# Kernel optimization log

Measured on AMD Instinct MI355X. Metric: run time of the kernel, lower is better.

## Reference

```python
import jax, jax.numpy as jnp
import numpy as np


def setup_inputs() -> dict:
    key = jax.random.key(0)
    k1, k2 = jax.random.split(key)
    N, D, K = 131072, 256, 1024
    x = jax.random.normal(k1, (N, D), dtype=jnp.float32)
    centroids = jax.random.normal(k2, (K, D), dtype=jnp.float32)
    return {"x": x, "centroids": centroids}


def reference(x, centroids):
    """Nearest-centroid assignment with euclidean similarity (kmeans_pytorch euc_sim):
        sim[n,k] = 2 * x[n] . c[k] - |x[n]|^2 - |c[k]|^2  ( = -||x[n]-c[k]||^2 )
    Returns (max_sim [N], labels [N]).
    """
    # [N, K] similarity via single GEMM plus broadcast norms
    sim = (2.0 * jnp.einsum('nd,kd->nk', x, centroids)
           - jnp.sum(x * x, axis=-1, keepdims=True)
           - jnp.sum(centroids * centroids, axis=-1)[None, :])
    max_sim = jnp.max(sim, axis=-1)
    labels = jnp.argmax(sim, axis=-1)
    return max_sim, labels
```

## Files before the change

kernel.cpp:

```cpp
#include <hip/hip_runtime.h>

constexpr int N = 131072;
constexpr int D = 256;
constexpr int K = 1024;

constexpr int TM = 128;
constexpr int TK = 128;
constexpr float EPS = 0.08f;

typedef _Float16 f16x8 __attribute__((ext_vector_type(8)));
typedef float f32x4 __attribute__((ext_vector_type(4)));

__device__ _Float16 g_ctile[66 * 8192];

__device__ __forceinline__ float sqf(float a) { return __fmul_rn(a, a); }

__device__ __forceinline__ float np_sumsq128(const float* q) {
    float lane[16];
#pragma unroll
    for (int j = 0; j < 16; j++) {
        const float r0 = __fadd_rn(sqf(q[j]),      sqf(q[64 + j]));
        const float r1 = __fadd_rn(sqf(q[16 + j]), sqf(q[80 + j]));
        const float r2 = __fadd_rn(sqf(q[32 + j]), sqf(q[96 + j]));
        const float r3 = __fadd_rn(sqf(q[48 + j]), sqf(q[112 + j]));
        lane[j] = __fadd_rn(__fadd_rn(r0, r1), __fadd_rn(r2, r3));
    }
    float t[8];
#pragma unroll
    for (int i = 0; i < 8; i++) t[i] = __fadd_rn(lane[i], lane[i + 8]);
    float u[4];
#pragma unroll
    for (int i = 0; i < 4; i++) u[i] = __fadd_rn(t[i], t[i + 4]);
    return __fadd_rn(__fadd_rn(u[0], u[2]), __fadd_rn(u[1], u[3]));
}
__device__ __forceinline__ float np_pw256_sq(const float* p) {
    return __fadd_rn(np_sumsq128(p), np_sumsq128(p + 128));
}

__device__ __forceinline__ float np_dot256(const float* a, const float* b) {
    float A[4] = {0.f, 0.f, 0.f, 0.f};
#pragma unroll 4
    for (int t = 0; t < 16; t++) {
#pragma unroll
        for (int i = 3; i >= 0; i--) {
            const int base = 16 * t + 4 * i;
#pragma unroll
            for (int j = 0; j < 4; j++)
                A[j] = __fadd_rn(A[j], __fmul_rn(a[base + j], b[base + j]));
        }
    }
    return __fadd_rn(__fadd_rn(A[0], A[1]), __fadd_rn(A[2], A[3]));
}

#define SPL(vec, comp, he, le, idx)                                  \
    {                                                                \
        const float fv_ = (vec).comp;                                \
        const _Float16 hh_ = (_Float16)fv_;                          \
        he[idx] = hh_;                                               \
        le[idx] = (_Float16)(fv_ - (float)hh_);                      \
    }

__global__ __launch_bounds__(256) void prep_kernel(const float* __restrict__ c,
                                                   float* __restrict__ cn) {
    const int idx = blockIdx.x * 256 + threadIdx.x;
    const int kglob = idx >> 5;
    const int dslot = idx & 31;
    const int dc = dslot >> 2, kg = dslot & 3;
    const float* src = c + (size_t)kglob * D + dc * 32 + kg * 8;
    const float4 s0 = ((const float4*)src)[0];
    const float4 s1 = ((const float4*)src)[1];
    f16x8 h, l;
    SPL(s0, x, h, l, 0) SPL(s0, y, h, l, 1) SPL(s0, z, h, l, 2) SPL(s0, w, h, l, 3)
    SPL(s1, x, h, l, 4) SPL(s1, y, h, l, 5) SPL(s1, z, h, l, 6) SPL(s1, w, h, l, 7)
    const int kblk = kglob >> 7, krow = kglob & 127;
    const int st = kblk * 8 + dc;
    _Float16* base = g_ctile + (size_t)st * 8192;
    *(f16x8*)&base[kg * 1024 + krow * 8]        = h;
    *(f16x8*)&base[4096 + kg * 1024 + krow * 8] = l;
    if (idx < K) cn[idx] = np_pw256_sq(c + (size_t)idx * D);
}

#define WAITVM(n) asm volatile("s_waitcnt vmcnt(" #n ")" ::: "memory")

__global__ __launch_bounds__(256, 2) void fast_kernel(const float* __restrict__ x,
                                                      const float* __restrict__ c,
                                                      const float* __restrict__ cn,
                                                      float* __restrict__ out,
                                                      int* __restrict__ cnt,
                                                      int* __restrict__ list) {
    __shared__ _Float16 cs[4][8192] __attribute__((aligned(16)));
    __shared__ float cn_sh[K];
    __shared__ float xn_sh[TM];
    __shared__ int   rbi[TM];
    __shared__ int   rok[TM];

    const int t    = threadIdx.x;
    const int n0   = blockIdx.x * TM;
    const int lane = t & 63;
    const int w    = t >> 6;
    const int wrow = w * 32;
    const int lr   = lane & 15;
    const int lg   = lane >> 4;

    const int kbR = blockIdx.x & 7;
    const int dcR = (blockIdx.x >> 3) & 7;
#define PHYS(p_) ((p_) < 64 ? (((((p_) >> 3) + kbR) & 7) << 3) | ((((p_) & 7) + dcR) & 7) : (p_))

#define STAGE(buf_, sidx_)                                                          \
    {                                                                               \
        const _Float16* gp_ = g_ctile + (size_t)(sidx_) * 8192 + t * 8;             \
        _Float16* lp_ = &cs[buf_][t * 8];                                           \
        _Pragma("unroll")                                                           \
        for (int u_ = 0; u_ < 4; u_++)                                              \
            __builtin_amdgcn_global_load_lds(                                       \
                (const __attribute__((address_space(1))) void*)(gp_ + u_ * 2048),   \
                (__attribute__((address_space(3))) void*)(lp_ + u_ * 2048),         \
                16, 0, 0);                                                          \
    }

    STAGE(0, PHYS(0));
    STAGE(1, PHYS(1));

#pragma unroll
    for (int q = 0; q < 4; q++) cn_sh[t + 256 * q] = cn[t + 256 * q];
    if (t < TM) xn_sh[t] = np_pw256_sq(x + (size_t)(n0 + t) * D);

    f16x8 ah[2][8], al[2][8];
#pragma unroll
    for (int st = 0; st < 8; st++) {
        const int pst = (st + dcR) & 7;
#pragma unroll
        for (int i = 0; i < 2; i++) {
            const float* src = x + (size_t)(n0 + wrow + 16 * i + lr) * D + pst * 32 + lg * 8;
            const float4 s0 = ((const float4*)src)[0];
            const float4 s1 = ((const float4*)src)[1];
            f16x8 h, l;
            SPL(s0, x, h, l, 0) SPL(s0, y, h, l, 1) SPL(s0, z, h, l, 2) SPL(s0, w, h, l, 3)
            SPL(s1, x, h, l, 4) SPL(s1, y, h, l, 5) SPL(s1, z, h, l, 6) SPL(s1, w, h, l, 7)
            ah[i][st] = h; al[i][st] = l;
        }
    }

    float v1[8], v2[8];
    int   i1[8];
#pragma unroll
    for (int s = 0; s < 8; s++) {
        v1[s] = -__builtin_inff(); v2[s] = -__builtin_inff(); i1[s] = 0;
    }

    __syncthreads();

    for (int kb0 = 0; kb0 < 8; kb0++) {
        const int kbE = (kb0 + kbR) & 7;
        f32x4 acc[2][8];
#pragma unroll
        for (int i = 0; i < 2; i++)
#pragma unroll
            for (int j = 0; j < 8; j++) acc[i][j] = (f32x4)(0.f);

#pragma unroll
        for (int dc8 = 0; dc8 < 8; dc8++) {
            const int p2 = kb0 * 8 + dc8 + 2;
            STAGE((dc8 + 2) & 3, PHYS(p2));
            WAITVM(8);
            __builtin_amdgcn_s_barrier();
            __builtin_amdgcn_sched_barrier(0);
            asm volatile("" ::: "memory");

            const _Float16* csb = &cs[dc8 & 3][0];
            __builtin_amdgcn_s_setprio(1);
#pragma unroll
            for (int j = 0; j < 8; j++) {
                const f16x8 bh = *(const f16x8*)&csb[lg * 1024 + (16 * j + lr) * 8];
                const f16x8 bl = *(const f16x8*)&csb[4096 + lg * 1024 + (16 * j + lr) * 8];
                acc[0][j] = __builtin_amdgcn_mfma_f32_16x16x32_f16(ah[0][dc8], bh, acc[0][j], 0, 0, 0);
                acc[1][j] = __builtin_amdgcn_mfma_f32_16x16x32_f16(ah[1][dc8], bh, acc[1][j], 0, 0, 0);
                acc[0][j] = __builtin_amdgcn_mfma_f32_16x16x32_f16(al[0][dc8], bh, acc[0][j], 0, 0, 0);
                acc[1][j] = __builtin_amdgcn_mfma_f32_16x16x32_f16(al[1][dc8], bh, acc[1][j], 0, 0, 0);
                acc[0][j] = __builtin_amdgcn_mfma_f32_16x16x32_f16(ah[0][dc8], bl, acc[0][j], 0, 0, 0);
                acc[1][j] = __builtin_amdgcn_mfma_f32_16x16x32_f16(ah[1][dc8], bl, acc[1][j], 0, 0, 0);
            }
            __builtin_amdgcn_s_setprio(0);
            asm volatile("" ::: "memory");
        }

#pragma unroll
        for (int j = 0; j < 8; j++) {
            const int kg_ = kbE * TK + 16 * j + lr;
            const float cnj = cn_sh[kg_];
#pragma unroll
            for (int i = 0; i < 2; i++)
#pragma unroll
                for (int r = 0; r < 4; r++) {
                    const int s = 4 * i + r;
                    const float v = 2.0f * acc[i][j][r] - xn_sh[wrow + 16 * i + 4 * lg + r] - cnj;
                    if (v > v1[s])       { v2[s] = v1[s]; v1[s] = v; i1[s] = kg_; }
                    else if (v > v2[s])  { v2[s] = v; }
                    else if (v == v1[s]) { v2[s] = v; }
                }
        }
    }

#pragma unroll
    for (int i = 0; i < 2; i++)
#pragma unroll
        for (int r = 0; r < 4; r++) {
            const int s = 4 * i + r;
            float a1v = v1[s], a2v = v2[s];
            int   ai  = i1[s];
#pragma unroll
            for (int m = 1; m <= 8; m <<= 1) {
                const float ov1 = __shfl_xor(a1v, m);
                const int   oi  = __shfl_xor(ai, m);
                const float ov2 = __shfl_xor(a2v, m);
                if (ov1 > a1v)      { a2v = fmaxf(a1v, ov2); a1v = ov1; ai = oi; }
                else if (ov1 < a1v) { a2v = fmaxf(a2v, ov1); }
                else                { ai = min(ai, oi); a2v = a1v; }
            }
            if (lr == 0) {
                const int row = wrow + 16 * i + 4 * lg + r;
                const int ok = (a1v - a2v >= EPS) ? 1 : 0;
                rbi[row] = ai;
                rok[row] = ok;
                if (!ok) { const int pos = atomicAdd(cnt, 1); list[pos] = n0 + row; }
            }
        }
    __syncthreads();

    if (t < TM && rok[t]) {
        const int row = n0 + t;
        const int bi  = rbi[t];
        const float dot = np_dot256(x + (size_t)row * D, c + (size_t)bi * D);
        const float v = __fsub_rn(__fsub_rn(__fmul_rn(2.0f, dot), xn_sh[t]), cn[bi]);
        out[row]     = v;
        out[N + row] = (float)bi;
    }
}

__global__ __launch_bounds__(256) void fallback_kernel(const float* __restrict__ x,
                                                       const float* __restrict__ c,
                                                       const float* __restrict__ cn,
                                                       float* __restrict__ out,
                                                       const int* __restrict__ cnt,
                                                       const int* __restrict__ list) {
    __shared__ float xrow[D];
    __shared__ float xn_s;
    __shared__ float wv[4];
    __shared__ int   wi[4];
    const int tid = threadIdx.x, lane = tid & 63, w = tid >> 6;
    const int total = *cnt;
    for (int idx = blockIdx.x; idx < total; idx += gridDim.x) {
        const int row = list[idx];
        if (tid < 64) *(float4*)&xrow[4 * tid] = ((const float4*)(x + (size_t)row * D))[tid];
        __syncthreads();
        if (tid == 0) xn_s = np_pw256_sq(xrow);
        __syncthreads();
        const float xn = xn_s;
        float bv = -__builtin_inff();
        int   bi = 0;
#pragma unroll
        for (int j = 0; j < 4; j++) {
            const int k = 4 * tid + j;
            const float dot = np_dot256(xrow, c + (size_t)k * D);
            const float v = __fsub_rn(__fsub_rn(__fmul_rn(2.0f, dot), xn), cn[k]);
            if (v > bv) { bv = v; bi = k; }
        }
#pragma unroll
        for (int m = 1; m <= 32; m <<= 1) {
            const float ov = __shfl_xor(bv, m);
            const int   oi = __shfl_xor(bi, m);
            if (ov > bv || (ov == bv && oi < bi)) { bv = ov; bi = oi; }
        }
        if (lane == 0) { wv[w] = bv; wi[w] = bi; }
        __syncthreads();
        if (tid == 0) {
#pragma unroll
            for (int ww = 1; ww < 4; ww++) {
                if (wv[ww] > bv || (wv[ww] == bv && wi[ww] < bi)) { bv = wv[ww]; bi = wi[ww]; }
            }
            out[row]     = bv;
            out[N + row] = (float)bi;
        }
        __syncthreads();
    }
}

extern "C" void kernel_launch(void* const* d_in, const int* in_sizes, int n_in,
                              void* d_out, int out_size, void* d_ws, size_t ws_size,
                              hipStream_t stream) {
    const float* x = (const float*)d_in[0];
    const float* c = (const float*)d_in[1];
    float* out     = (float*)d_out;
    float* cn = (float*)d_ws;
    int* cnt  = (int*)((char*)d_ws + 4096);
    int* list = (int*)((char*)d_ws + 4608);

    hipMemsetAsync(cnt, 0, sizeof(int), stream);
    prep_kernel<<<128, 256, 0, stream>>>(c, cn);
    fast_kernel<<<N / TM, 256, 0, stream>>>(x, c, cn, out, cnt, list);
    fallback_kernel<<<1024, 256, 0, stream>>>(x, c, cn, out, cnt, list);
}
```

Measured before the change: 562.8 us.

## Use 512-thread blocks with 16 rows per wave to cut register use

Each block now runs 8 waves instead of 4, and each wave owns 16 rows rather than 32. That halves the per-thread A fragments, accumulators and top-2 state, and the launch bounds ask for 4 blocks per CU. Per-thread staging loads drop from 4 to 2, and the wait count is adjusted to match. The goal is higher occupancy and better latency hiding. The cost is that each B fragment read from LDS now feeds only half as many MFMAs, which doubles LDS read traffic per unit of work, and more waves take part in each barrier.

```diff
diff --git a/kernel.cpp b/kernel.cpp
--- a/kernel.cpp
+++ b/kernel.cpp
@@ -82,7 +82,7 @@
 
 #define WAITVM(n) asm volatile("s_waitcnt vmcnt(" #n ")" ::: "memory")
 
-__global__ __launch_bounds__(256, 2) void fast_kernel(const float* __restrict__ x,
+__global__ __launch_bounds__(512, 4) void fast_kernel(const float* __restrict__ x,
                                                       const float* __restrict__ c,
                                                       const float* __restrict__ cn,
                                                       float* __restrict__ out,
@@ -98,7 +98,7 @@
     const int n0   = blockIdx.x * TM;
     const int lane = t & 63;
     const int w    = t >> 6;
-    const int wrow = w * 32;
+    const int wrow = w * 16;
     const int lr   = lane & 15;
     const int lg   = lane >> 4;
 
@@ -110,41 +110,38 @@
     {                                                                               \
         const _Float16* gp_ = g_ctile + (size_t)(sidx_) * 8192 + t * 8;             \
         _Float16* lp_ = &cs[buf_][t * 8];                                           \
-        _Pragma("unroll")                                                           \
-        for (int u_ = 0; u_ < 4; u_++)                                              \
-            __builtin_amdgcn_global_load_lds(                                       \
-                (const __attribute__((address_space(1))) void*)(gp_ + u_ * 2048),   \
-                (__attribute__((address_space(3))) void*)(lp_ + u_ * 2048),         \
-                16, 0, 0);                                                          \
+        __builtin_amdgcn_global_load_lds(                                           \
+            (const __attribute__((address_space(1))) void*)gp_,                     \
+            (__attribute__((address_space(3))) void*)lp_, 16, 0, 0);                \
+        __builtin_amdgcn_global_load_lds(                                           \
+            (const __attribute__((address_space(1))) void*)(gp_ + 4096),            \
+            (__attribute__((address_space(3))) void*)(lp_ + 4096), 16, 0, 0);       \
     }
 
     STAGE(0, PHYS(0));
     STAGE(1, PHYS(1));
 
 #pragma unroll
-    for (int q = 0; q < 4; q++) cn_sh[t + 256 * q] = cn[t + 256 * q];
+    for (int q = 0; q < 2; q++) cn_sh[t + 512 * q] = cn[t + 512 * q];
     if (t < TM) xn_sh[t] = np_pw256_sq(x + (size_t)(n0 + t) * D);
 
-    f16x8 ah[2][8], al[2][8];
+    f16x8 ah[8], al[8];
 #pragma unroll
     for (int st = 0; st < 8; st++) {
         const int pst = (st + dcR) & 7;
-#pragma unroll
-        for (int i = 0; i < 2; i++) {
-            const float* src = x + (size_t)(n0 + wrow + 16 * i + lr) * D + pst * 32 + lg * 8;
-            const float4 s0 = ((const float4*)src)[0];
-            const float4 s1 = ((const float4*)src)[1];
-            f16x8 h, l;
-            SPL(s0, x, h, l, 0) SPL(s0, y, h, l, 1) SPL(s0, z, h, l, 2) SPL(s0, w, h, l, 3)
-            SPL(s1, x, h, l, 4) SPL(s1, y, h, l, 5) SPL(s1, z, h, l, 6) SPL(s1, w, h, l, 7)
-            ah[i][st] = h; al[i][st] = l;
-        }
-    }
-
-    float v1[8], v2[8];
-    int   i1[8];
-#pragma unroll
-    for (int s = 0; s < 8; s++) {
+        const float* src = x + (size_t)(n0 + wrow + lr) * D + pst * 32 + lg * 8;
+        const float4 s0 = ((const float4*)src)[0];
+        const float4 s1 = ((const float4*)src)[1];
+        f16x8 h, l;
+        SPL(s0, x, h, l, 0) SPL(s0, y, h, l, 1) SPL(s0, z, h, l, 2) SPL(s0, w, h, l, 3)
+        SPL(s1, x, h, l, 4) SPL(s1, y, h, l, 5) SPL(s1, z, h, l, 6) SPL(s1, w, h, l, 7)
+        ah[st] = h; al[st] = l;
+    }
+
+    float v1[4], v2[4];
+    int   i1[4];
+#pragma unroll
+    for (int s = 0; s < 4; s++) {
         v1[s] = -__builtin_inff(); v2[s] = -__builtin_inff(); i1[s] = 0;
     }
 
@@ -152,17 +149,15 @@
 
     for (int kb0 = 0; kb0 < 8; kb0++) {
         const int kbE = (kb0 + kbR) & 7;
-        f32x4 acc[2][8];
-#pragma unroll
-        for (int i = 0; i < 2; i++)
-#pragma unroll
-            for (int j = 0; j < 8; j++) acc[i][j] = (f32x4)(0.f);
+        f32x4 acc[8];
+#pragma unroll
+        for (int j = 0; j < 8; j++) acc[j] = (f32x4)(0.f);
 
 #pragma unroll
         for (int dc8 = 0; dc8 < 8; dc8++) {
             const int p2 = kb0 * 8 + dc8 + 2;
             STAGE((dc8 + 2) & 3, PHYS(p2));
-            WAITVM(8);
+            WAITVM(4);
             __builtin_amdgcn_s_barrier();
             __builtin_amdgcn_sched_barrier(0);
             asm volatile("" ::: "memory");
@@ -173,12 +168,9 @@
             for (int j = 0; j < 8; j++) {
                 const f16x8 bh = *(const f16x8*)&csb[lg * 1024 + (16 * j + lr) * 8];
                 const f16x8 bl = *(const f16x8*)&csb[4096 + lg * 1024 + (16 * j + lr) * 8];
-                acc[0][j] = __builtin_amdgcn_mfma_f32_16x16x32_f16(ah[0][dc8], bh, acc[0][j], 0, 0, 0);
-                acc[1][j] = __builtin_amdgcn_mfma_f32_16x16x32_f16(ah[1][dc8], bh, acc[1][j], 0, 0, 0);
-                acc[0][j] = __builtin_amdgcn_mfma_f32_16x16x32_f16(al[0][dc8], bh, acc[0][j], 0, 0, 0);
-                acc[1][j] = __builtin_amdgcn_mfma_f32_16x16x32_f16(al[1][dc8], bh, acc[1][j], 0, 0, 0);
-                acc[0][j] = __builtin_amdgcn_mfma_f32_16x16x32_f16(ah[0][dc8], bl, acc[0][j], 0, 0, 0);
-                acc[1][j] = __builtin_amdgcn_mfma_f32_16x16x32_f16(ah[1][dc8], bl, acc[1][j], 0, 0, 0);
+                acc[j] = __builtin_amdgcn_mfma_f32_16x16x32_f16(ah[dc8], bh, acc[j], 0, 0, 0);
+                acc[j] = __builtin_amdgcn_mfma_f32_16x16x32_f16(al[dc8], bh, acc[j], 0, 0, 0);
+                acc[j] = __builtin_amdgcn_mfma_f32_16x16x32_f16(ah[dc8], bl, acc[j], 0, 0, 0);
             }
             __builtin_amdgcn_s_setprio(0);
             asm volatile("" ::: "memory");
@@ -189,42 +181,36 @@
             const int kg_ = kbE * TK + 16 * j + lr;
             const float cnj = cn_sh[kg_];
 #pragma unroll
-            for (int i = 0; i < 2; i++)
-#pragma unroll
-                for (int r = 0; r < 4; r++) {
-                    const int s = 4 * i + r;
-                    const float v = 2.0f * acc[i][j][r] - xn_sh[wrow + 16 * i + 4 * lg + r] - cnj;
-                    if (v > v1[s])       { v2[s] = v1[s]; v1[s] = v; i1[s] = kg_; }
-                    else if (v > v2[s])  { v2[s] = v; }
-                    else if (v == v1[s]) { v2[s] = v; }
-                }
-        }
-    }
-
-#pragma unroll
-    for (int i = 0; i < 2; i++)
-#pragma unroll
-        for (int r = 0; r < 4; r++) {
-            const int s = 4 * i + r;
-            float a1v = v1[s], a2v = v2[s];
-            int   ai  = i1[s];
-#pragma unroll
-            for (int m = 1; m <= 8; m <<= 1) {
-                const float ov1 = __shfl_xor(a1v, m);
-                const int   oi  = __shfl_xor(ai, m);
-                const float ov2 = __shfl_xor(a2v, m);
-                if (ov1 > a1v)      { a2v = fmaxf(a1v, ov2); a1v = ov1; ai = oi; }
-                else if (ov1 < a1v) { a2v = fmaxf(a2v, ov1); }
-                else                { ai = min(ai, oi); a2v = a1v; }
+            for (int r = 0; r < 4; r++) {
+                const float v = 2.0f * acc[j][r] - xn_sh[wrow + 4 * lg + r] - cnj;
+                if (v > v1[r])       { v2[r] = v1[r]; v1[r] = v; i1[r] = kg_; }
+                else if (v > v2[r])  { v2[r] = v; }
+                else if (v == v1[r]) { v2[r] = v; }
             }
-            if (lr == 0) {
-                const int row = wrow + 16 * i + 4 * lg + r;
-                const int ok = (a1v - a2v >= EPS) ? 1 : 0;
-                rbi[row] = ai;
-                rok[row] = ok;
-                if (!ok) { const int pos = atomicAdd(cnt, 1); list[pos] = n0 + row; }
-            }
-        }
+        }
+    }
+
+#pragma unroll
+    for (int r = 0; r < 4; r++) {
+        float a1v = v1[r], a2v = v2[r];
+        int   ai  = i1[r];
+#pragma unroll
+        for (int m = 1; m <= 8; m <<= 1) {
+            const float ov1 = __shfl_xor(a1v, m);
+            const int   oi  = __shfl_xor(ai, m);
+            const float ov2 = __shfl_xor(a2v, m);
+            if (ov1 > a1v)      { a2v = fmaxf(a1v, ov2); a1v = ov1; ai = oi; }
+            else if (ov1 < a1v) { a2v = fmaxf(a2v, ov1); }
+            else                { ai = min(ai, oi); a2v = a1v; }
+        }
+        if (lr == 0) {
+            const int row = wrow + 4 * lg + r;
+            const int ok = (a1v - a2v >= EPS) ? 1 : 0;
+            rbi[row] = ai;
+            rok[row] = ok;
+            if (!ok) { const int pos = atomicAdd(cnt, 1); list[pos] = n0 + row; }
+        }
+    }
     __syncthreads();
 
     if (t < TM && rok[t]) {
@@ -297,6 +283,6 @@
 
     hipMemsetAsync(cnt, 0, sizeof(int), stream);
     prep_kernel<<<128, 256, 0, stream>>>(c, cn);
-    fast_kernel<<<N / TM, 256, 0, stream>>>(x, c, cn, out, cnt, list);
+    fast_kernel<<<N / TM, 512, 0, stream>>>(x, c, cn, out, cnt, list);
     fallback_kernel<<<1024, 256, 0, stream>>>(x, c, cn, out, cnt, list);
 }
```

Result: faster. 534.7 us (-5.0%).
